# Optimization experiments

Hardware: AMD Instinct MI355X
Metric: run time of the kernel (lower is better)

The kernel has to match this reference:

```python
import jax, jax.numpy as jnp
import numpy as np

MARGIN = 1.0
EPS = 1e-6


def _cos(a, b):
    # Row-wise cosine similarity, matching torch.nn.CosineSimilarity semantics:
    # dot / max(||a|| * ||b||, eps)
    num = jnp.sum(a * b, axis=-1)
    den = jnp.maximum(jnp.linalg.norm(a, axis=-1) * jnp.linalg.norm(b, axis=-1), EPS)
    return num / den


def setup_inputs() -> dict:
    key = jax.random.key(0)
    k1, k2, k3 = jax.random.split(key, 3)
    B, D = 16384, 1024
    output = jax.random.normal(k1, (B, D), dtype=jnp.float32)
    target = jax.random.normal(k2, (B, D), dtype=jnp.float32)
    # offset in [0, B-1); j = (i + 1 + neg_idx) % B guarantees j != i, uniform over the rest
    neg_idx = jax.random.randint(k3, (B,), 0, B - 1, dtype=jnp.int64)
    return {"output": output, "target": target, "neg_idx": neg_idx}


def reference(output, target, neg_idx):
    B = output.shape[0]
    j = (jnp.arange(B) + 1 + neg_idx) % B  # random negative index, j != i
    t_neg = target[j]                       # gather negative label embeddings [B, D]
    hinge = jax.nn.relu(MARGIN - _cos(target, output) + _cos(t_neg, output))
    return jnp.sum(hinge) / B
```

## Files before the change

kernel.cpp:

```cpp
#include <hip/hip_runtime.h>
#include <hip/hip_bf16.h>


#define EPS 1e-6f

typedef float f4 __attribute__((ext_vector_type(4)));

#define DPP_STEP(x, ctrl, rm, bm)                                             \
    x += __int_as_float(__builtin_amdgcn_update_dpp(                          \
        0, __float_as_int(x), (ctrl), (rm), (bm), true))

__device__ __forceinline__ float dpp_wave_sum(float x) {
    DPP_STEP(x, 0x111, 0xf, 0xf);
    DPP_STEP(x, 0x112, 0xf, 0xf);
    DPP_STEP(x, 0x114, 0xf, 0xe);
    DPP_STEP(x, 0x118, 0xf, 0xc);
    DPP_STEP(x, 0x142, 0xa, 0xf);
    DPP_STEP(x, 0x143, 0xc, 0xf);
    return x;
}

struct RowBuf {
    f4 o[4], t[4], n[4];
};

__device__ __forceinline__ void issue_loads(RowBuf& rb,
                                            const float* __restrict__ outm,
                                            const float* __restrict__ tgt,
                                            int i, int j, int lane, int D) {
    const f4* o4 = (const f4*)(outm + (size_t)i * D);
    const f4* t4 = (const f4*)(tgt  + (size_t)i * D);
    const f4* n4 = (const f4*)(tgt  + (size_t)j * D);
#pragma unroll
    for (int k = 0; k < 4; ++k)
        rb.o[k] = __builtin_nontemporal_load(&o4[lane + 64 * k]);
#pragma unroll
    for (int k = 0; k < 4; ++k) rb.t[k] = t4[lane + 64 * k];
#pragma unroll
    for (int k = 0; k < 4; ++k) rb.n[k] = n4[lane + 64 * k];
}

__device__ __forceinline__ float consume(const RowBuf& rb) {
    float dto = 0.f, dno = 0.f, oo = 0.f, tt = 0.f, nn = 0.f;
#pragma unroll
    for (int k = 0; k < 4; ++k) {
        dto += rb.o[k].x*rb.t[k].x + rb.o[k].y*rb.t[k].y + rb.o[k].z*rb.t[k].z + rb.o[k].w*rb.t[k].w;
        dno += rb.o[k].x*rb.n[k].x + rb.o[k].y*rb.n[k].y + rb.o[k].z*rb.n[k].z + rb.o[k].w*rb.n[k].w;
        oo  += rb.o[k].x*rb.o[k].x + rb.o[k].y*rb.o[k].y + rb.o[k].z*rb.o[k].z + rb.o[k].w*rb.o[k].w;
        tt  += rb.t[k].x*rb.t[k].x + rb.t[k].y*rb.t[k].y + rb.t[k].z*rb.t[k].z + rb.t[k].w*rb.t[k].w;
        nn  += rb.n[k].x*rb.n[k].x + rb.n[k].y*rb.n[k].y + rb.n[k].z*rb.n[k].z + rb.n[k].w*rb.n[k].w;
    }
    dto = dpp_wave_sum(dto);
    dno = dpp_wave_sum(dno);
    oo  = dpp_wave_sum(oo);
    tt  = dpp_wave_sum(tt);
    nn  = dpp_wave_sum(nn);
    float no = sqrtf(oo);
    float h  = 1.f - dto / fmaxf(sqrtf(tt) * no, EPS)
                   + dno / fmaxf(sqrtf(nn) * no, EPS);
    return fmaxf(h, 0.f);
}

__global__ __launch_bounds__(256, 4) void hinge_cos_kernel(
    const float* __restrict__ outm,
    const float* __restrict__ tgt,
    const int*   __restrict__ negidx,
    float* __restrict__ res,
    int B, int D, float invB) {

    const int lane  = threadIdx.x & 63;
    const int wave  = threadIdx.x >> 6;
    const int wpb   = blockDim.x >> 6;
    const int gwave = blockIdx.x * wpb + wave;
    const int nwav  = gridDim.x * wpb;

    float acc = 0.f;

    RowBuf cur, nxt;
    int i = gwave;
    if (i < B) {
        int j = i + 1 + negidx[i];
        if (j >= B) j -= B;
        issue_loads(cur, outm, tgt, i, j, lane, D);
    }
    while (i < B) {
        const int inext = i + nwav;
        const bool havenext = inext < B;
        if (havenext) {
            int jn = inext + 1 + negidx[inext];
            if (jn >= B) jn -= B;
            issue_loads(nxt, outm, tgt, inext, jn, lane, D);
        }
        float h = consume(cur);
        if (lane == 63) acc += h;
        if (havenext) cur = nxt;
        i = inext;
    }

    __shared__ float red[4];
    if (lane == 63) red[wave] = acc;
    __syncthreads();
    if (threadIdx.x == 0) {
        float s = 0.f;
#pragma unroll
        for (int w = 0; w < 4; ++w) s += red[w];
        atomicAdd(res, s * invB);
    }
}

extern "C" void kernel_launch(void* const* d_in, const int* in_sizes, int n_in,
                              void* d_out, int out_size, void* d_ws, size_t ws_size,
                              hipStream_t stream) {
    const float* outm   = (const float*)d_in[0];
    const float* tgt    = (const float*)d_in[1];
    const int*   negidx = (const int*)d_in[2];
    float* res = (float*)d_out;

    const int B = in_sizes[2];
    const int D = in_sizes[0] / B;

    (void)hipMemsetAsync(res, 0, sizeof(float), stream);

    hinge_cos_kernel<<<1024, 256, 0, stream>>>(outm, tgt, negidx, res, B, D,
                                               1.0f / (float)B);
}
```

Baseline: 142.4 us.

## Replace persistent double-buffered loop with one-row-per-wave grid

Drops the persistent grid-stride loop with software double buffering and launches one wave per row, B/4 blocks in total, relying on higher occupancy (launch bounds raised to 8 blocks per SM) to hide memory latency. The nontemporal hint on the output loads is also removed. Each block now issues its own atomicAdd, which raises atomic traffic from 1024 to 4096 adds on a single address and adds more block launch overhead.

```diff
diff --git a/kernel.cpp b/kernel.cpp
--- a/kernel.cpp
+++ b/kernel.cpp
@@ -1,5 +1,4 @@
 #include <hip/hip_runtime.h>
-#include <hip/hip_bf16.h>
 
 
 #define EPS 1e-6f
@@ -20,90 +19,60 @@
     return x;
 }
 
-struct RowBuf {
-    f4 o[4], t[4], n[4];
-};
-
-__device__ __forceinline__ void issue_loads(RowBuf& rb,
-                                            const float* __restrict__ outm,
-                                            const float* __restrict__ tgt,
-                                            int i, int j, int lane, int D) {
-    const f4* o4 = (const f4*)(outm + (size_t)i * D);
-    const f4* t4 = (const f4*)(tgt  + (size_t)i * D);
-    const f4* n4 = (const f4*)(tgt  + (size_t)j * D);
-#pragma unroll
-    for (int k = 0; k < 4; ++k)
-        rb.o[k] = __builtin_nontemporal_load(&o4[lane + 64 * k]);
-#pragma unroll
-    for (int k = 0; k < 4; ++k) rb.t[k] = t4[lane + 64 * k];
-#pragma unroll
-    for (int k = 0; k < 4; ++k) rb.n[k] = n4[lane + 64 * k];
-}
-
-__device__ __forceinline__ float consume(const RowBuf& rb) {
-    float dto = 0.f, dno = 0.f, oo = 0.f, tt = 0.f, nn = 0.f;
-#pragma unroll
-    for (int k = 0; k < 4; ++k) {
-        dto += rb.o[k].x*rb.t[k].x + rb.o[k].y*rb.t[k].y + rb.o[k].z*rb.t[k].z + rb.o[k].w*rb.t[k].w;
-        dno += rb.o[k].x*rb.n[k].x + rb.o[k].y*rb.n[k].y + rb.o[k].z*rb.n[k].z + rb.o[k].w*rb.n[k].w;
-        oo  += rb.o[k].x*rb.o[k].x + rb.o[k].y*rb.o[k].y + rb.o[k].z*rb.o[k].z + rb.o[k].w*rb.o[k].w;
-        tt  += rb.t[k].x*rb.t[k].x + rb.t[k].y*rb.t[k].y + rb.t[k].z*rb.t[k].z + rb.t[k].w*rb.t[k].w;
-        nn  += rb.n[k].x*rb.n[k].x + rb.n[k].y*rb.n[k].y + rb.n[k].z*rb.n[k].z + rb.n[k].w*rb.n[k].w;
-    }
-    dto = dpp_wave_sum(dto);
-    dno = dpp_wave_sum(dno);
-    oo  = dpp_wave_sum(oo);
-    tt  = dpp_wave_sum(tt);
-    nn  = dpp_wave_sum(nn);
-    float no = sqrtf(oo);
-    float h  = 1.f - dto / fmaxf(sqrtf(tt) * no, EPS)
-                   + dno / fmaxf(sqrtf(nn) * no, EPS);
-    return fmaxf(h, 0.f);
-}
-
-__global__ __launch_bounds__(256, 4) void hinge_cos_kernel(
+__global__ __launch_bounds__(256, 8) void hinge_cos_kernel(
     const float* __restrict__ outm,
     const float* __restrict__ tgt,
     const int*   __restrict__ negidx,
     float* __restrict__ res,
     int B, int D, float invB) {
 
-    const int lane  = threadIdx.x & 63;
-    const int wave  = threadIdx.x >> 6;
-    const int wpb   = blockDim.x >> 6;
-    const int gwave = blockIdx.x * wpb + wave;
-    const int nwav  = gridDim.x * wpb;
+    const int lane = threadIdx.x & 63;
+    const int wave = threadIdx.x >> 6;
+    const int i    = blockIdx.x * 4 + wave;
 
-    float acc = 0.f;
+    float h = 0.f;
+    if (i < B) {
+        const int g = negidx[i];
 
-    RowBuf cur, nxt;
-    int i = gwave;
-    if (i < B) {
-        int j = i + 1 + negidx[i];
-        if (j >= B) j -= B;
-        issue_loads(cur, outm, tgt, i, j, lane, D);
-    }
-    while (i < B) {
-        const int inext = i + nwav;
-        const bool havenext = inext < B;
-        if (havenext) {
-            int jn = inext + 1 + negidx[inext];
-            if (jn >= B) jn -= B;
-            issue_loads(nxt, outm, tgt, inext, jn, lane, D);
+        const f4* o4 = (const f4*)(outm + (size_t)i * D);
+        const f4* t4 = (const f4*)(tgt  + (size_t)i * D);
+
+        f4 o[4], t[4], n[4];
+#pragma unroll
+        for (int k = 0; k < 4; ++k) o[k] = o4[lane + 64 * k];
+#pragma unroll
+        for (int k = 0; k < 4; ++k) t[k] = t4[lane + 64 * k];
+
+        int j = i + 1 + g; if (j >= B) j -= B;
+        const f4* n4 = (const f4*)(tgt + (size_t)j * D);
+#pragma unroll
+        for (int k = 0; k < 4; ++k) n[k] = n4[lane + 64 * k];
+
+        float dto = 0.f, dno = 0.f, oo = 0.f, tt = 0.f, nn = 0.f;
+#pragma unroll
+        for (int k = 0; k < 4; ++k) {
+            dto += o[k].x*t[k].x + o[k].y*t[k].y + o[k].z*t[k].z + o[k].w*t[k].w;
+            dno += o[k].x*n[k].x + o[k].y*n[k].y + o[k].z*n[k].z + o[k].w*n[k].w;
+            oo  += o[k].x*o[k].x + o[k].y*o[k].y + o[k].z*o[k].z + o[k].w*o[k].w;
+            tt  += t[k].x*t[k].x + t[k].y*t[k].y + t[k].z*t[k].z + t[k].w*t[k].w;
+            nn  += n[k].x*n[k].x + n[k].y*n[k].y + n[k].z*n[k].z + n[k].w*n[k].w;
         }
-        float h = consume(cur);
-        if (lane == 63) acc += h;
-        if (havenext) cur = nxt;
-        i = inext;
+        dto = dpp_wave_sum(dto);
+        dno = dpp_wave_sum(dno);
+        oo  = dpp_wave_sum(oo);
+        tt  = dpp_wave_sum(tt);
+        nn  = dpp_wave_sum(nn);
+        float no = sqrtf(oo);
+        float hv = 1.f - dto / fmaxf(sqrtf(tt) * no, EPS)
+                       + dno / fmaxf(sqrtf(nn) * no, EPS);
+        h = fmaxf(hv, 0.f);
     }
 
     __shared__ float red[4];
-    if (lane == 63) red[wave] = acc;
+    if (lane == 63) red[wave] = h;
     __syncthreads();
     if (threadIdx.x == 0) {
-        float s = 0.f;
-#pragma unroll
-        for (int w = 0; w < 4; ++w) s += red[w];
+        float s = red[0] + red[1] + red[2] + red[3];
         atomicAdd(res, s * invB);
     }
 }
@@ -121,6 +90,7 @@
 
     (void)hipMemsetAsync(res, 0, sizeof(float), stream);
 
-    hinge_cos_kernel<<<1024, 256, 0, stream>>>(outm, tgt, negidx, res, B, D,
-                                               1.0f / (float)B);
+    const int blocks = (B + 3) / 4;
+    hinge_cos_kernel<<<blocks, 256, 0, stream>>>(outm, tgt, negidx, res, B, D,
+                                                 1.0f / (float)B);
 }
```

New measurement: 172.4 us. 1.21x slower.
